# Performance work log

Measured on AMD Instinct MI355X. Metric: run time of the kernel, lower is better.

Reference implementation:

```python
import jax, jax.numpy as jnp
import numpy as np

B, N, K, TC = 4, 4096, 16, 3
N_TAYLOR = 20  # 3rd-order Taylor monomials of (x,y,z): 1 + 3 + 6 + 10
CHANNELS = [(6, 32), (32, 64), (64, 128), (128, 256)]


def _taylor(rel):
    # rel: B,3,N,K relative coords -> B,20,N,K monomial basis up to degree 3
    x, y, z = rel[:, 0], rel[:, 1], rel[:, 2]
    one = jnp.ones_like(x)
    return jnp.stack([one, x, y, z,
                      x * x, x * y, x * z, y * y, y * z, z * z,
                      x * x * x, x * x * y, x * x * z, x * y * y, x * y * z,
                      x * z * z, y * y * y, y * y * z, y * z * z, z * z * z], axis=1)


def _group(feat, idx):
    # feat: B,C,N ; idx: B,N,K (int) -> B,C,N,K gathered neighbor features
    return jax.vmap(lambda f, i: f[:, i])(feat, idx)


def setup_inputs() -> dict:
    key = jax.random.key(0)
    ks = jax.random.split(key, 8)
    inp = {"pc": jax.random.normal(ks[0], (B, N, 6), dtype=jnp.float32)}
    for l, (cin, cout) in enumerate(CHANNELS, start=1):
        k1, k2 = jax.random.split(ks[l], 2)
        inp[f"w1_{l}"] = jax.random.normal(k1, (TC, N_TAYLOR), dtype=jnp.float32) * 0.1
        inp[f"b1_{l}"] = jnp.zeros((TC,), dtype=jnp.float32)
        fan_in = cin * TC * K
        inp[f"w2_{l}"] = jax.random.normal(k2, (cout, cin * TC, K), dtype=jnp.float32) * (1.0 / np.sqrt(fan_in))
        inp[f"b2_{l}"] = jnp.zeros((cout,), dtype=jnp.float32)
    return inp


def _forward(pc, params):
    pcT = pc.transpose(0, 2, 1)                 # B,6,N
    xyz = pcT[:, :3]                            # B,3,N
    # KNN graph: pairwise squared distances, top-k nearest (includes self)
    sq = jnp.sum(xyz * xyz, axis=1)             # B,N
    d2 = sq[:, :, None] + sq[:, None, :] - 2.0 * jnp.einsum('bcn,bcm->bnm', xyz, xyz)
    _, idx = jax.lax.top_k(-d2, K)              # B,N,K
    gxyz = _group(xyz, idx)                     # B,3,N,K
    rel = gxyz - xyz[:, :, :, None]             # B,3,N,K relative neighbor coords
    tay_basis = _taylor(rel)                    # B,20,N,K

    feat = pcT
    feats = []
    for (w1, b1, w2, b2) in params:
        # Taylor kernel weights: 1x1 conv over the 20 monomials -> TC channels
        tay = jnp.einsum('btnk,ct->bcnk', tay_basis, w1) + b1[None, :, None, None]  # B,TC,N,K
        gf = _group(feat, idx)                  # B,C,N,K
        C = gf.shape[1]
        fused = (gf[:, :, None] * tay[:, None]).reshape(B, C * TC, N, K)  # outer product
        # Conv2d(C*TC, out, kernel=(1,K)): contract channel and neighbor axes
        out = jnp.einsum('bcnk,ock->bon', fused, w2) + b2[None, :, None]
        feat = jax.nn.relu(out)                 # B,Cout,N
        feats.append(feat)

    point_feat = jnp.concatenate(feats, axis=1)  # B,480,N
    top2, _ = jax.lax.top_k(point_feat, 2)       # top-2 over N (last axis) -> B,480,2
    cat_feat = top2.reshape(B, -1)               # B,960
    return cat_feat, point_feat


def reference(pc, w1_1, b1_1, w2_1, b2_1, w1_2, b1_2, w2_2, b2_2,
              w1_3, b1_3, w2_3, b2_3, w1_4, b1_4, w2_4, b2_4):
    params = [(w1_1, b1_1, w2_1, b2_1), (w1_2, b1_2, w2_2, b2_2),
              (w1_3, b1_3, w2_3, b2_3), (w1_4, b1_4, w2_4, b2_4)]
    return _forward(pc, params)
```

## Files before the change

kernel.cpp:

```cpp
#include <hip/hip_runtime.h>
#include <hip/hip_fp16.h>
#include <cfloat>

#define BB 4
#define NN 4096
#define KK 16
#define NPTS (BB * NN)

typedef __attribute__((ext_vector_type(8))) _Float16 f16x8;
typedef __attribute__((ext_vector_type(4))) float f32x4;
typedef unsigned int u32;
typedef unsigned long long u64;

__device__ __forceinline__ short f2h(float v) {
  __half h = __float2half_rn(v);
  return __half_as_short(h);
}
__device__ __forceinline__ u32 mulh2(u32 a, __half2 t) {
  __half2 x = __hmul2(*(__half2*)&a, t);
  return *(u32*)&x;
}

__device__ __forceinline__ void wcvt_body(const float* __restrict__ w2,
                                          short* __restrict__ wb,
                                          int CIN, int COUT, int CPAD, int LOGC,
                                          int total8, int i) {
  if (i >= total8) return;
  const int q8 = i * 8;
  const int QT = CPAD * 48;
  const int o = q8 / QT;
  const int r = q8 - o * QT;
  const int kq = r >> LOGC;
  const int c0 = r & (CPAD - 1);
  const int tt = kq >> 4;
  const int k = kq & 15;
  short h[8];
#pragma unroll
  for (int j = 0; j < 8; ++j) {
    const int c = c0 + j;
    const float v = (o < COUT && c < CIN) ? w2[(size_t)o * CIN * 48 + (c * 3 + tt) * 16 + k] : 0.0f;
    h[j] = f2h(v);
  }
  short* d = wb + (size_t)o * QT + r;
#pragma unroll
  for (int j = 0; j < 8; ++j) d[j] = h[j];
}

__global__ __launch_bounds__(256) void prep_kernel(
    const float* __restrict__ pc, short* __restrict__ ft0, float4* __restrict__ xyzq,
    const float* __restrict__ w2_1, short* __restrict__ wb1,
    const float* __restrict__ w2_2, short* __restrict__ wb2,
    const float* __restrict__ w2_3, short* __restrict__ wb3,
    const float* __restrict__ w2_4, short* __restrict__ wb4) {
  const int blk = blockIdx.x;
  const int t = threadIdx.x;
  if (blk < 64) {
    const int i = blk * 256 + t;
    const float* s = pc + (size_t)i * 6;
    short* d = ft0 + (size_t)i * 8;
#pragma unroll
    for (int c = 0; c < 6; ++c) d[c] = f2h(s[c]);
    d[6] = 0; d[7] = 0;
    const float x = s[0], y = s[1], z = s[2];
    xyzq[i] = make_float4(x, y, z, fmaf(z, z, fmaf(y, y, x * x)));
  } else if (blk < 76) {
    wcvt_body(w2_1, wb1, 6, 32, 8, 3, 3072, (blk - 64) * 256 + t);
  } else if (blk < 124) {
    wcvt_body(w2_2, wb2, 32, 64, 32, 5, 12288, (blk - 76) * 256 + t);
  } else if (blk < 316) {
    wcvt_body(w2_3, wb3, 64, 128, 64, 6, 49152, (blk - 124) * 256 + t);
  } else {
    wcvt_body(w2_4, wb4, 128, 256, 128, 7, 196608, (blk - 316) * 256 + t);
  }
}

__global__ __launch_bounds__(256) void knn_select2(const float4* __restrict__ xyzq,
                                                   int* __restrict__ idx_out) {
  __shared__ float wT[2][4];
  __shared__ u64 list[2][128];
  __shared__ int lcnt[2];
  const int g0 = blockIdx.x * 2;
  const int b = g0 >> 12;
  const int t = threadIdx.x;
  const int lane = t & 63;
  const float4* base = xyzq + (b << 12);
  const float4 qa = xyzq[g0];
  const float4 qb = xyzq[g0 + 1];
  float da[16], db[16];
  float mina = FLT_MAX, minb = FLT_MAX;
#pragma unroll
  for (int i = 0; i < 16; ++i) {
    const float4 c = base[i * 256 + t];
    const float dota = fmaf(qa.z, c.z, fmaf(qa.y, c.y, qa.x * c.x));
    da[i] = fmaf(-2.0f, dota, qa.w + c.w);
    mina = fminf(mina, da[i]);
    const float dotb = fmaf(qb.z, c.z, fmaf(qb.y, c.y, qb.x * c.x));
    db[i] = fmaf(-2.0f, dotb, qb.w + c.w);
    minb = fminf(minb, db[i]);
  }
  if (t < 2) lcnt[t] = 0;
  float va = mina, vb = minb;
#pragma unroll
  for (int k = 2; k <= 64; k <<= 1) {
#pragma unroll
    for (int j = k >> 1; j >= 1; j >>= 1) {
      const float oa = __shfl_xor(va, j, 64);
      const float ob = __shfl_xor(vb, j, 64);
      const bool take_min = (((lane & k) == 0) == ((lane & j) == 0));
      va = take_min ? fminf(va, oa) : fmaxf(va, oa);
      vb = take_min ? fminf(vb, ob) : fmaxf(vb, ob);
    }
  }
  const float twa = __shfl(va, 15, 64);
  const float twb = __shfl(vb, 15, 64);
  if (lane == 0) { wT[0][t >> 6] = twa; wT[1][t >> 6] = twb; }
  __syncthreads();
  const float Ta = fminf(fminf(wT[0][0], wT[0][1]), fminf(wT[0][2], wT[0][3]));
  const float Tb = fminf(fminf(wT[1][0], wT[1][1]), fminf(wT[1][2], wT[1][3]));
#pragma unroll
  for (int i = 0; i < 16; ++i) {
    if (da[i] <= Ta) {
      const u32 bits = __float_as_uint(da[i]);
      const u32 key = bits ^ ((u32)((int)bits >> 31) | 0x80000000u);
      const int pos = atomicAdd(&lcnt[0], 1);
      if (pos < 128) list[0][pos] = ((u64)key << 32) | (u32)(i * 256 + t);
    }
    if (db[i] <= Tb) {
      const u32 bits = __float_as_uint(db[i]);
      const u32 key = bits ^ ((u32)((int)bits >> 31) | 0x80000000u);
      const int pos = atomicAdd(&lcnt[1], 1);
      if (pos < 128) list[1][pos] = ((u64)key << 32) | (u32)(i * 256 + t);
    }
  }
  __syncthreads();
  if (t < 128) {
#pragma unroll
    for (int qq = 0; qq < 2; ++qq) {
      const int m = min(lcnt[qq], 128);
      const u64 my = (t < m) ? list[qq][t] : ~0ull;
      int rank = 0;
#pragma unroll 4
      for (int i = 0; i < m; ++i) rank += (list[qq][i] < my) ? 1 : 0;
      if (t < m && rank < 16)
        idx_out[(size_t)(g0 + qq) * KK + rank] = (int)(my & 0xFFFFFFFFull);
    }
  }
}

template <int CPAD, int LOGC, int COUT, int OTILE>
__global__ __launch_bounds__(256) void conv_mfma_kernel(
    const char* __restrict__ ftin,
    const short* __restrict__ wb,
    const float* __restrict__ b2,
    const float4* __restrict__ xyzq,
    const float* __restrict__ w1,
    const float* __restrict__ b1,
    const int* __restrict__ idx,
    float* __restrict__ pfout, int pfbstride,
    short* __restrict__ ftout, int CPADN) {
  constexpr int QTOT = CPAD * 48;
  constexpr int OUTER = QTOT / 64;
  constexpr int NJ = OTILE / 64;
  constexpr int NJC = (NJ == 2) ? 4 : 1;
  constexpr int NH = OTILE / 32;
  __shared__ __align__(16) short As[2][OTILE * 64];
  __shared__ __align__(16) short Bs[2][64 * 64];
  __shared__ __align__(16) unsigned short tayH[48 * 64];
  __shared__ int idxS[16 * 64];
  const int t = threadIdx.x;
  const int pbase = blockIdx.x * 64;
  const int obase = blockIdx.y * OTILE;
  const int b = pbase >> 12;
  const int nbase = pbase & (NN - 1);
  const int p_loc = t >> 2;
  const int sub = t & 3;
  {
    const int4 mi = *(const int4*)&idx[(size_t)(pbase + p_loc) * KK + sub * 4];
    const int gb = b << 12;
    idxS[(sub * 4 + 0) * 64 + p_loc] = (gb + mi.x) << (LOGC + 1);
    idxS[(sub * 4 + 1) * 64 + p_loc] = (gb + mi.y) << (LOGC + 1);
    idxS[(sub * 4 + 2) * 64 + p_loc] = (gb + mi.z) << (LOGC + 1);
    idxS[(sub * 4 + 3) * 64 + p_loc] = (gb + mi.w) << (LOGC + 1);
    const float4 self = xyzq[pbase + p_loc];
    const int nbr[4] = {gb + mi.x, gb + mi.y, gb + mi.z, gb + mi.w};
#pragma unroll
    for (int j = 0; j < 4; ++j) {
      const float4 nb = xyzq[nbr[j]];
      const float x = nb.x - self.x;
      const float y = nb.y - self.y;
      const float z = nb.z - self.z;
      float tb[20];
      tb[0] = 1.0f; tb[1] = x; tb[2] = y; tb[3] = z;
      tb[4] = x * x; tb[5] = x * y; tb[6] = x * z;
      tb[7] = y * y; tb[8] = y * z; tb[9] = z * z;
      tb[10] = tb[4] * x; tb[11] = tb[4] * y; tb[12] = tb[4] * z;
      tb[13] = tb[5] * y; tb[14] = tb[5] * z; tb[15] = tb[6] * z;
      tb[16] = tb[7] * y; tb[17] = tb[7] * z; tb[18] = tb[8] * z; tb[19] = tb[9] * z;
      const int k = sub * 4 + j;
#pragma unroll
      for (int c = 0; c < 3; ++c) {
        float s = b1[c];
#pragma unroll
        for (int jj = 0; jj < 20; ++jj) s = fmaf(w1[c * 20 + jj], tb[jj], s);
        tayH[(c * 16 + k) * 64 + p_loc] = (unsigned short)f2h(s);
      }
    }
  }
  const int arow = t >> 3;
  const int apos = t & 7;
  const int aswz = (t >> 4) & 7;
  const short* awl[NH];
#pragma unroll
  for (int h = 0; h < NH; ++h)
    awl[h] = wb + (size_t)(obase + h * 32 + arow) * QTOT + ((apos ^ aswz) * 8);
  auto dmaA = [&](int o, int ph) {
#pragma unroll
    for (int h = 0; h < NH; ++h)
      __builtin_amdgcn_global_load_lds(
          (const __attribute__((address_space(1))) u32*)(awl[h] + o * 64),
          (__attribute__((address_space(3))) u32*)&As[ph][h * 2048 + t * 8], 16, 0, 0);
  };
  const int lane = t & 63;
  const int w = t >> 6;
  const int wm = (NJ == 2) ? (w & 1) : 0;
  const int ksw = (NJ == 2) ? (w >> 1) : 0;
  const int wn = (NJ == 2) ? 0 : w;
  const int fr = lane & 15;
  const int fk = lane >> 4;
  const int rsw = (fr >> 1) & 7;
  const int bswz = (p_loc >> 1) & 7;
  f32x4 acc[4][NJC];
#pragma unroll
  for (int i = 0; i < 4; ++i)
#pragma unroll
    for (int j = 0; j < NJC; ++j) acc[i][j] = (f32x4)(0.0f);

  uint4 fv[2];
  unsigned short tvh[2];
  auto prefB = [&](int o) {
#pragma unroll
    for (int z = 0; z < 2; ++z) {
      const int q0 = o * 64 + z * 32 + sub * 8;
      const int kq = q0 >> LOGC;
      const int c0 = q0 & (CPAD - 1);
      const int moff = idxS[(kq & 15) * 64 + p_loc];
      tvh[z] = tayH[kq * 64 + p_loc];
      fv[z] = *(const uint4*)(ftin + moff + (c0 << 1));
    }
  };
  auto buildB = [&](int ph) {
#pragma unroll
    for (int z = 0; z < 2; ++z) {
      const __half2 t2 = __half2half2(__ushort_as_half(tvh[z]));
      const uint4 f = fv[z];
      uint4 r;
      r.x = mulh2(f.x, t2); r.y = mulh2(f.y, t2);
      r.z = mulh2(f.z, t2); r.w = mulh2(f.w, t2);
      const int pos = (z * 4 + sub) ^ bswz;
      *(uint4*)&Bs[ph][p_loc * 64 + pos * 8] = r;
    }
  };
  dmaA(0, 0);
  __syncthreads();
  prefB(0);
  buildB(0);
  __syncthreads();
#pragma unroll 1
  for (int o = 0; o < OUTER; ++o) {
    const int ph = o & 1;
    if (o + 1 < OUTER) { dmaA(o + 1, ph ^ 1); prefB(o + 1); }
    if constexpr (NJ == 2) {
      f16x8 af[4], bf[4];
      const int pos8 = ((ksw * 4 + fk) ^ rsw) * 8;
#pragma unroll
      for (int i = 0; i < 4; ++i)
        af[i] = *(const f16x8*)&As[ph][(wm * 64 + i * 16 + fr) * 64 + pos8];
#pragma unroll
      for (int j = 0; j < 4; ++j)
        bf[j] = *(const f16x8*)&Bs[ph][(j * 16 + fr) * 64 + pos8];
#pragma unroll
      for (int i = 0; i < 4; ++i)
#pragma unroll
        for (int j = 0; j < 4; ++j)
          acc[i][j] = __builtin_amdgcn_mfma_f32_16x16x32_f16(af[i], bf[j], acc[i][j], 0, 0, 0);
      if (o + 1 < OUTER) buildB(ph ^ 1);
    } else {
#pragma unroll
      for (int z = 0; z < 2; ++z) {
        f16x8 af[4], bf;
        const int pos8 = ((z * 4 + fk) ^ rsw) * 8;
#pragma unroll
        for (int i = 0; i < 4; ++i)
          af[i] = *(const f16x8*)&As[ph][(i * 16 + fr) * 64 + pos8];
        bf = *(const f16x8*)&Bs[ph][(wn * 16 + fr) * 64 + pos8];
#pragma unroll
        for (int i = 0; i < 4; ++i)
          acc[i][0] = __builtin_amdgcn_mfma_f32_16x16x32_f16(af[i], bf, acc[i][0], 0, 0, 0);
      }
      if (o + 1 < OUTER) buildB(ph ^ 1);
    }
    if (o + 1 < OUTER) __syncthreads();
  }
  if constexpr (NJ == 2) {
    __syncthreads();
    float* red = (float*)(&As[0][0]) + wm * 4096;
    if (ksw == 1) {
#pragma unroll
      for (int i = 0; i < 4; ++i)
#pragma unroll
        for (int j = 0; j < 4; ++j)
#pragma unroll
          for (int r = 0; r < 4; ++r)
            red[((i * 4 + j) * 4 + r) * 64 + lane] = acc[i][j][r];
    }
    __syncthreads();
    if (ksw == 1) return;
#pragma unroll
    for (int i = 0; i < 4; ++i)
#pragma unroll
      for (int j = 0; j < 4; ++j)
#pragma unroll
        for (int r = 0; r < 4; ++r)
          acc[i][j][r] += red[((i * 4 + j) * 4 + r) * 64 + lane];
  }
  float* outb = pfout + (size_t)b * pfbstride;
#pragma unroll
  for (int i = 0; i < 4; ++i) {
    const int o0 = obase + wm * 64 + i * 16 + fk * 4;
    if (o0 < COUT) {
      const float4 b4 = *(const float4*)&b2[o0];
#pragma unroll
      for (int j = 0; j < NJC; ++j) {
        const int p_l = (NJ == 2) ? (j * 16 + fr) : (wn * 16 + fr);
        const float v0 = fmaxf(acc[i][j][0] + b4.x, 0.0f);
        const float v1 = fmaxf(acc[i][j][1] + b4.y, 0.0f);
        const float v2 = fmaxf(acc[i][j][2] + b4.z, 0.0f);
        const float v3 = fmaxf(acc[i][j][3] + b4.w, 0.0f);
        outb[(size_t)(o0 + 0) * NN + nbase + p_l] = v0;
        outb[(size_t)(o0 + 1) * NN + nbase + p_l] = v1;
        outb[(size_t)(o0 + 2) * NN + nbase + p_l] = v2;
        outb[(size_t)(o0 + 3) * NN + nbase + p_l] = v3;
        if (ftout) {
          const __half2 h01 = __floats2half2_rn(v0, v1);
          const __half2 h23 = __floats2half2_rn(v2, v3);
          uint2 pk;
          pk.x = *(const u32*)&h01;
          pk.y = *(const u32*)&h23;
          *(uint2*)&ftout[(size_t)(pbase + p_l) * CPADN + o0] = pk;
        }
      }
    }
  }
}

__global__ __launch_bounds__(256) void top2_kernel(const float* __restrict__ pf,
                                                   float* __restrict__ cat) {
  const int row = blockIdx.x;
  const float* p = pf + (size_t)row * NN;
  float m1 = -FLT_MAX, m2 = -FLT_MAX;
  for (int i = threadIdx.x; i < NN; i += 256) {
    const float v = p[i];
    if (v > m1) { m2 = m1; m1 = v; }
    else if (v > m2) m2 = v;
  }
#pragma unroll
  for (int off = 32; off > 0; off >>= 1) {
    const float o1 = __shfl_down(m1, off, 64);
    const float o2 = __shfl_down(m2, off, 64);
    const float nm1 = fmaxf(m1, o1);
    const float nm2 = fmaxf(fminf(m1, o1), fmaxf(m2, o2));
    m1 = nm1; m2 = nm2;
  }
  __shared__ float s1[4], s2[4];
  const int wid = threadIdx.x >> 6;
  if ((threadIdx.x & 63) == 0) { s1[wid] = m1; s2[wid] = m2; }
  __syncthreads();
  if (threadIdx.x == 0) {
    m1 = s1[0]; m2 = s2[0];
#pragma unroll
    for (int w = 1; w < 4; ++w) {
      const float o1 = s1[w], o2 = s2[w];
      const float nm1 = fmaxf(m1, o1);
      const float nm2 = fmaxf(fminf(m1, o1), fmaxf(m2, o2));
      m1 = nm1; m2 = nm2;
    }
    const int b = row / 480, ch = row % 480;
    cat[b * 960 + ch * 2 + 0] = m1;
    cat[b * 960 + ch * 2 + 1] = m2;
  }
}

extern "C" void kernel_launch(void* const* d_in, const int* in_sizes, int n_in,
                              void* d_out, int out_size, void* d_ws, size_t ws_size,
                              hipStream_t stream) {
  const float* pc = (const float*)d_in[0];
  const float* w1s[4]; const float* b1s[4]; const float* w2s[4]; const float* b2s[4];
  for (int l = 0; l < 4; ++l) {
    w1s[l] = (const float*)d_in[1 + 4 * l];
    b1s[l] = (const float*)d_in[2 + 4 * l];
    w2s[l] = (const float*)d_in[3 + 4 * l];
    b2s[l] = (const float*)d_in[4 + 4 * l];
  }
  char* W = (char*)d_ws;
  int* idx = (int*)W;
  float4* xyzq = (float4*)(W + 1048576);
  short* wb1 = (short*)(W + 1310720);
  short* wb2 = (short*)(W + 1359872);
  short* wb3 = (short*)(W + 1556480);
  short* wb4 = (short*)(W + 2342912);
  short* ft0 = (short*)(W + 5488640);
  short* ft1 = (short*)(W + 5750784);
  short* ft2 = (short*)(W + 6799360);
  short* ft3 = (short*)(W + 8896512);
  float* cat = (float*)d_out;
  float* pf = (float*)d_out + BB * 960;
  const int pfstride = 480 * NN;

  prep_kernel<<<dim3(1084), 256, 0, stream>>>(
      pc, ft0, xyzq, w2s[0], wb1, w2s[1], wb2, w2s[2], wb3, w2s[3], wb4);
  knn_select2<<<dim3(NPTS / 2), 256, 0, stream>>>(xyzq, idx);
  conv_mfma_kernel<8, 3, 32, 64><<<dim3(NPTS / 64, 1), 256, 0, stream>>>(
      (const char*)ft0, wb1, b2s[0], xyzq, w1s[0], b1s[0], idx,
      pf + (size_t)0 * NN, pfstride, ft1, 32);
  conv_mfma_kernel<32, 5, 64, 64><<<dim3(NPTS / 64, 1), 256, 0, stream>>>(
      (const char*)ft1, wb2, b2s[1], xyzq, w1s[1], b1s[1], idx,
      pf + (size_t)32 * NN, pfstride, ft2, 64);
  conv_mfma_kernel<64, 6, 128, 64><<<dim3(NPTS / 64, 2), 256, 0, stream>>>(
      (const char*)ft2, wb3, b2s[2], xyzq, w1s[2], b1s[2], idx,
      pf + (size_t)96 * NN, pfstride, ft3, 128);
  conv_mfma_kernel<128, 7, 256, 128><<<dim3(NPTS / 64, 2), 256, 0, stream>>>(
      (const char*)ft3, wb4, b2s[3], xyzq, w1s[3], b1s[3], idx,
      pf + (size_t)224 * NN, pfstride, nullptr, 0);
  top2_kernel<<<dim3(BB * 480), 256, 0, stream>>>(pf, cat);
}
```

Before: 334.1 us.

## Split conv reduction dimension across two blocks with flag-based partial-sum handoff

Each conv layer grid gains a z dimension of 2, and each block reduces half of the CPAD*48 contraction (24 of the 48 taylor-neighbor rows). The first block to finish stores raw partial sums to the output. The second spins on a global flag, then adds its partials plus bias, applies ReLU and writes the fp16 features. Neighbor indices in shared memory shrink to 16-bit, and the taylor table is halved. The aim is more parallelism and occupancy for the small-grid layers. The cost is an extra global read/write pass, a memset and a spin-wait, which could deadlock if the second block becomes resident before the first.

```diff
diff --git a/kernel.cpp b/kernel.cpp
--- a/kernel.cpp
+++ b/kernel.cpp
@@ -156,20 +156,24 @@
     const float* __restrict__ w1,
     const float* __restrict__ b1,
     const int* __restrict__ idx,
+    int* __restrict__ flags,
     float* __restrict__ pfout, int pfbstride,
     short* __restrict__ ftout, int CPADN) {
   constexpr int QTOT = CPAD * 48;
-  constexpr int OUTER = QTOT / 64;
+  constexpr int OUTER = QTOT / 128;
   constexpr int NJ = OTILE / 64;
   constexpr int NJC = (NJ == 2) ? 4 : 1;
   constexpr int NH = OTILE / 32;
   __shared__ __align__(16) short As[2][OTILE * 64];
   __shared__ __align__(16) short Bs[2][64 * 64];
-  __shared__ __align__(16) unsigned short tayH[48 * 64];
-  __shared__ int idxS[16 * 64];
+  __shared__ __align__(16) unsigned short tayH[24 * 64];
+  __shared__ unsigned short idxS[16 * 64];
+  __shared__ int sOld;
   const int t = threadIdx.x;
   const int pbase = blockIdx.x * 64;
   const int obase = blockIdx.y * OTILE;
+  const int bz = blockIdx.z;
+  const int kzoff = 24 * bz;
   const int b = pbase >> 12;
   const int nbase = pbase & (NN - 1);
   const int p_loc = t >> 2;
@@ -177,10 +181,10 @@
   {
     const int4 mi = *(const int4*)&idx[(size_t)(pbase + p_loc) * KK + sub * 4];
     const int gb = b << 12;
-    idxS[(sub * 4 + 0) * 64 + p_loc] = (gb + mi.x) << (LOGC + 1);
-    idxS[(sub * 4 + 1) * 64 + p_loc] = (gb + mi.y) << (LOGC + 1);
-    idxS[(sub * 4 + 2) * 64 + p_loc] = (gb + mi.z) << (LOGC + 1);
-    idxS[(sub * 4 + 3) * 64 + p_loc] = (gb + mi.w) << (LOGC + 1);
+    idxS[(sub * 4 + 0) * 64 + p_loc] = (unsigned short)(gb + mi.x);
+    idxS[(sub * 4 + 1) * 64 + p_loc] = (unsigned short)(gb + mi.y);
+    idxS[(sub * 4 + 2) * 64 + p_loc] = (unsigned short)(gb + mi.z);
+    idxS[(sub * 4 + 3) * 64 + p_loc] = (unsigned short)(gb + mi.w);
     const float4 self = xyzq[pbase + p_loc];
     const int nbr[4] = {gb + mi.x, gb + mi.y, gb + mi.z, gb + mi.w};
 #pragma unroll
@@ -202,7 +206,9 @@
         float s = b1[c];
 #pragma unroll
         for (int jj = 0; jj < 20; ++jj) s = fmaf(w1[c * 20 + jj], tb[jj], s);
-        tayH[(c * 16 + k) * 64 + p_loc] = (unsigned short)f2h(s);
+        const int kq = c * 16 + k;
+        if (kq >= kzoff && kq < kzoff + 24)
+          tayH[(kq - kzoff) * 64 + p_loc] = (unsigned short)f2h(s);
       }
     }
   }
@@ -212,7 +218,8 @@
   const short* awl[NH];
 #pragma unroll
   for (int h = 0; h < NH; ++h)
-    awl[h] = wb + (size_t)(obase + h * 32 + arow) * QTOT + ((apos ^ aswz) * 8);
+    awl[h] = wb + (size_t)(obase + h * 32 + arow) * QTOT + ((apos ^ aswz) * 8)
+               + (size_t)bz * (QTOT / 2);
   auto dmaA = [&](int o, int ph) {
 #pragma unroll
     for (int h = 0; h < NH; ++h)
@@ -241,10 +248,11 @@
 #pragma unroll
     for (int z = 0; z < 2; ++z) {
       const int q0 = o * 64 + z * 32 + sub * 8;
-      const int kq = q0 >> LOGC;
+      const int kql = q0 >> LOGC;
       const int c0 = q0 & (CPAD - 1);
-      const int moff = idxS[(kq & 15) * 64 + p_loc];
-      tvh[z] = tayH[kq * 64 + p_loc];
+      const int kidx = (kql + kzoff) & 15;
+      const int moff = ((int)idxS[kidx * 64 + p_loc]) << (LOGC + 1);
+      tvh[z] = tayH[kql * 64 + p_loc];
       fv[z] = *(const uint4*)(ftin + moff + (c0 << 1));
     }
   };
@@ -268,7 +276,7 @@
 #pragma unroll 1
   for (int o = 0; o < OUTER; ++o) {
     const int ph = o & 1;
-    if (o + 1 < OUTER) { dmaA(o + 1, ph ^ 1); prefB(o + 1); }
+    if (o + 1 < OUTER) { prefB(o + 1); dmaA(o + 1, ph ^ 1); }
     if constexpr (NJ == 2) {
       f16x8 af[4], bf[4];
       const int pos8 = ((ksw * 4 + fk) ^ rsw) * 8;
@@ -314,41 +322,74 @@
             red[((i * 4 + j) * 4 + r) * 64 + lane] = acc[i][j][r];
     }
     __syncthreads();
-    if (ksw == 1) return;
-#pragma unroll
-    for (int i = 0; i < 4; ++i)
-#pragma unroll
-      for (int j = 0; j < 4; ++j)
-#pragma unroll
-        for (int r = 0; r < 4; ++r)
-          acc[i][j][r] += red[((i * 4 + j) * 4 + r) * 64 + lane];
-  }
+    if (ksw == 0) {
+#pragma unroll
+      for (int i = 0; i < 4; ++i)
+#pragma unroll
+        for (int j = 0; j < 4; ++j)
+#pragma unroll
+          for (int r = 0; r < 4; ++r)
+            acc[i][j][r] += red[((i * 4 + j) * 4 + r) * 64 + lane];
+    }
+  }
+  int* flagp = flags + blockIdx.y * gridDim.x + blockIdx.x;
+  if (t == 0) sOld = atomicAdd(flagp, 1);
+  __syncthreads();
+  const bool first = (sOld == 0);
+  if (!first) {
+    if (t == 0) {
+      while (__hip_atomic_load(flagp, __ATOMIC_ACQUIRE, __HIP_MEMORY_SCOPE_AGENT) < 2)
+        __builtin_amdgcn_s_sleep(1);
+    }
+    __syncthreads();
+  }
+  const bool writer = (NJ == 2) ? (ksw == 0) : true;
   float* outb = pfout + (size_t)b * pfbstride;
-#pragma unroll
-  for (int i = 0; i < 4; ++i) {
-    const int o0 = obase + wm * 64 + i * 16 + fk * 4;
-    if (o0 < COUT) {
-      const float4 b4 = *(const float4*)&b2[o0];
-#pragma unroll
-      for (int j = 0; j < NJC; ++j) {
-        const int p_l = (NJ == 2) ? (j * 16 + fr) : (wn * 16 + fr);
-        const float v0 = fmaxf(acc[i][j][0] + b4.x, 0.0f);
-        const float v1 = fmaxf(acc[i][j][1] + b4.y, 0.0f);
-        const float v2 = fmaxf(acc[i][j][2] + b4.z, 0.0f);
-        const float v3 = fmaxf(acc[i][j][3] + b4.w, 0.0f);
-        outb[(size_t)(o0 + 0) * NN + nbase + p_l] = v0;
-        outb[(size_t)(o0 + 1) * NN + nbase + p_l] = v1;
-        outb[(size_t)(o0 + 2) * NN + nbase + p_l] = v2;
-        outb[(size_t)(o0 + 3) * NN + nbase + p_l] = v3;
-        if (ftout) {
-          const __half2 h01 = __floats2half2_rn(v0, v1);
-          const __half2 h23 = __floats2half2_rn(v2, v3);
-          uint2 pk;
-          pk.x = *(const u32*)&h01;
-          pk.y = *(const u32*)&h23;
-          *(uint2*)&ftout[(size_t)(pbase + p_l) * CPADN + o0] = pk;
+  if (writer) {
+#pragma unroll
+    for (int i = 0; i < 4; ++i) {
+      const int o0 = obase + wm * 64 + i * 16 + fk * 4;
+      if (o0 < COUT) {
+#pragma unroll
+        for (int j = 0; j < NJC; ++j) {
+          const int p_l = (NJ == 2) ? (j * 16 + fr) : (wn * 16 + fr);
+          if (first) {
+            outb[(size_t)(o0 + 0) * NN + nbase + p_l] = acc[i][j][0];
+            outb[(size_t)(o0 + 1) * NN + nbase + p_l] = acc[i][j][1];
+            outb[(size_t)(o0 + 2) * NN + nbase + p_l] = acc[i][j][2];
+            outb[(size_t)(o0 + 3) * NN + nbase + p_l] = acc[i][j][3];
+          } else {
+            const float4 b4 = *(const float4*)&b2[o0];
+            const float p0 = outb[(size_t)(o0 + 0) * NN + nbase + p_l];
+            const float p1 = outb[(size_t)(o0 + 1) * NN + nbase + p_l];
+            const float p2 = outb[(size_t)(o0 + 2) * NN + nbase + p_l];
+            const float p3 = outb[(size_t)(o0 + 3) * NN + nbase + p_l];
+            const float v0 = fmaxf(acc[i][j][0] + p0 + b4.x, 0.0f);
+            const float v1 = fmaxf(acc[i][j][1] + p1 + b4.y, 0.0f);
+            const float v2 = fmaxf(acc[i][j][2] + p2 + b4.z, 0.0f);
+            const float v3 = fmaxf(acc[i][j][3] + p3 + b4.w, 0.0f);
+            outb[(size_t)(o0 + 0) * NN + nbase + p_l] = v0;
+            outb[(size_t)(o0 + 1) * NN + nbase + p_l] = v1;
+            outb[(size_t)(o0 + 2) * NN + nbase + p_l] = v2;
+            outb[(size_t)(o0 + 3) * NN + nbase + p_l] = v3;
+            if (ftout) {
+              const __half2 h01 = __floats2half2_rn(v0, v1);
+              const __half2 h23 = __floats2half2_rn(v2, v3);
+              uint2 pk;
+              pk.x = *(const u32*)&h01;
+              pk.y = *(const u32*)&h23;
+              *(uint2*)&ftout[(size_t)(pbase + p_l) * CPADN + o0] = pk;
+            }
+          }
         }
       }
+    }
+  }
+  if (first) {
+    __syncthreads();
+    if (t == 0) {
+      __threadfence();
+      __hip_atomic_fetch_add(flagp, 1, __ATOMIC_RELEASE, __HIP_MEMORY_SCOPE_AGENT);
     }
   }
 }
@@ -412,24 +453,30 @@
   short* ft1 = (short*)(W + 5750784);
   short* ft2 = (short*)(W + 6799360);
   short* ft3 = (short*)(W + 8896512);
+  int* flags = (int*)(W + 13090816);
   float* cat = (float*)d_out;
   float* pf = (float*)d_out + BB * 960;
   const int pfstride = 480 * NN;
-
+  int* f1 = flags;
+  int* f2 = flags + 256;
+  int* f3 = flags + 512;
+  int* f4 = flags + 1024;
+
+  hipMemsetAsync(flags, 0, 1536 * sizeof(int), stream);
   prep_kernel<<<dim3(1084), 256, 0, stream>>>(
       pc, ft0, xyzq, w2s[0], wb1, w2s[1], wb2, w2s[2], wb3, w2s[3], wb4);
   knn_select2<<<dim3(NPTS / 2), 256, 0, stream>>>(xyzq, idx);
-  conv_mfma_kernel<8, 3, 32, 64><<<dim3(NPTS / 64, 1), 256, 0, stream>>>(
-      (const char*)ft0, wb1, b2s[0], xyzq, w1s[0], b1s[0], idx,
+  conv_mfma_kernel<8, 3, 32, 64><<<dim3(NPTS / 64, 1, 2), 256, 0, stream>>>(
+      (const char*)ft0, wb1, b2s[0], xyzq, w1s[0], b1s[0], idx, f1,
       pf + (size_t)0 * NN, pfstride, ft1, 32);
-  conv_mfma_kernel<32, 5, 64, 64><<<dim3(NPTS / 64, 1), 256, 0, stream>>>(
-      (const char*)ft1, wb2, b2s[1], xyzq, w1s[1], b1s[1], idx,
+  conv_mfma_kernel<32, 5, 64, 64><<<dim3(NPTS / 64, 1, 2), 256, 0, stream>>>(
+      (const char*)ft1, wb2, b2s[1], xyzq, w1s[1], b1s[1], idx, f2,
       pf + (size_t)32 * NN, pfstride, ft2, 64);
-  conv_mfma_kernel<64, 6, 128, 64><<<dim3(NPTS / 64, 2), 256, 0, stream>>>(
-      (const char*)ft2, wb3, b2s[2], xyzq, w1s[2], b1s[2], idx,
+  conv_mfma_kernel<64, 6, 128, 64><<<dim3(NPTS / 64, 2, 2), 256, 0, stream>>>(
+      (const char*)ft2, wb3, b2s[2], xyzq, w1s[2], b1s[2], idx, f3,
       pf + (size_t)96 * NN, pfstride, ft3, 128);
-  conv_mfma_kernel<128, 7, 256, 128><<<dim3(NPTS / 64, 2), 256, 0, stream>>>(
-      (const char*)ft3, wb4, b2s[3], xyzq, w1s[3], b1s[3], idx,
+  conv_mfma_kernel<128, 7, 256, 128><<<dim3(NPTS / 64, 2, 2), 256, 0, stream>>>(
+      (const char*)ft3, wb4, b2s[3], xyzq, w1s[3], b1s[3], idx, f4,
       pf + (size_t)224 * NN, pfstride, nullptr, 0);
   top2_kernel<<<dim3(BB * 480), 256, 0, stream>>>(pf, cat);
 }
```

Result: slower. 420.8 us (+26.0%).
